# Optimization experiments

Hardware: AMD Instinct MI355X
Metric: run time of the kernel (lower is better)

Reference implementation:

```python
import jax, jax.numpy as jnp
import numpy as np

B, V, P, D = 32, 6, 197, 512
L = 77          # CLIP token length
C = 5           # num quality perspectives (conditions)

def _normalize(x, axis=-1, eps=1e-12):
    n = jnp.linalg.norm(x, axis=axis, keepdims=True)
    return x / jnp.maximum(n, eps)

def _conv3x3(x, w, b):
    # x: [C,112,7,7], w: [O,112,3,3] -> [C,O,7,7]
    y = jax.lax.conv_general_dilated(x, w, (1, 1), 'SAME',
                                     dimension_numbers=('NCHW', 'OIHW', 'NCHW'))
    return y + b[None, :, None, None]

def setup_inputs() -> dict:
    key = jax.random.key(0)
    ks = jax.random.split(key, 20)
    s = 0.02  # weight init scale keeps sigmoids in linear-ish range
    return {
        'feature_texture': jax.random.normal(ks[0], (B, V * P, D), jnp.float32),
        'feature_prompt': jax.random.normal(ks[1], (B, L, D), jnp.float32),
        'feature_prompt_eot': jax.random.normal(ks[2], (B, D), jnp.float32),
        'feature_condition': jax.random.normal(ks[3], (C, D), jnp.float32),
        'fc_quality_w': jax.random.normal(ks[4], (224, D), jnp.float32) * s,
        'fc_quality_b': jnp.zeros((224,), jnp.float32),
        'fc_condition_w': jax.random.normal(ks[5], (5488, D), jnp.float32) * s,
        'fc_condition_b': jnp.zeros((5488,), jnp.float32),
        'fc1w_conv_w': jax.random.normal(ks[6], (512, 112, 3, 3), jnp.float32) * s,
        'fc1w_conv_b': jnp.zeros((512,), jnp.float32),
        'fc2w_conv_w': jax.random.normal(ks[7], (128, 112, 3, 3), jnp.float32) * s,
        'fc2w_conv_b': jnp.zeros((128,), jnp.float32),
        'fc3w_conv_w': jax.random.normal(ks[8], (32, 112, 3, 3), jnp.float32) * s,
        'fc3w_conv_b': jnp.zeros((32,), jnp.float32),
        'fc4w_conv_w': jax.random.normal(ks[9], (8, 112, 3, 3), jnp.float32) * s,
        'fc4w_conv_b': jnp.zeros((8,), jnp.float32),
        'fc1b_w': jax.random.normal(ks[10], (112, 112), jnp.float32) * s,
        'fc1b_b': jnp.zeros((112,), jnp.float32),
        'fc2b_w': jax.random.normal(ks[11], (56, 112), jnp.float32) * s,
        'fc2b_b': jnp.zeros((56,), jnp.float32),
        'fc3b_w': jax.random.normal(ks[12], (28, 112), jnp.float32) * s,
        'fc3b_b': jnp.zeros((28,), jnp.float32),
        'fc4b_w': jax.random.normal(ks[13], (14, 112), jnp.float32) * s,
        'fc4b_b': jnp.zeros((14,), jnp.float32),
        'fc5w_w': jax.random.normal(ks[14], (14, 112), jnp.float32) * s,
        'fc5w_b': jnp.zeros((14,), jnp.float32),
        'fc5b_w': jax.random.normal(ks[15], (1, 112), jnp.float32) * s,
        'fc5b_b': jnp.zeros((1,), jnp.float32),
    }

def reference(feature_texture, feature_prompt, feature_prompt_eot, feature_condition,
              fc_quality_w, fc_quality_b, fc_condition_w, fc_condition_b,
              fc1w_conv_w, fc1w_conv_b, fc2w_conv_w, fc2w_conv_b,
              fc3w_conv_w, fc3w_conv_b, fc4w_conv_w, fc4w_conv_b,
              fc1b_w, fc1b_b, fc2b_w, fc2b_b, fc3b_w, fc3b_b, fc4b_w, fc4b_b,
              fc5w_w, fc5w_b, fc5b_w, fc5b_b):
    nC = feature_condition.shape[0]

    # --- calculate_cos: mean of relu(pairwise cosine sim), upper triangle i<j ---
    fn = _normalize(feature_condition)                      # [C,512]
    gram = fn @ fn.T                                        # [C,C]
    iu, ju = jnp.triu_indices(nC, k=1)
    loss_dis = jnp.mean(jnp.maximum(gram[iu, ju], 0.0))

    # --- cross-attention-style patch weighting ---
    np_prompt = _normalize(feature_prompt, axis=2)          # [B,L,D]
    np_tex = _normalize(feature_texture, axis=2)            # [B,J,D]
    sim_texture = jnp.einsum('bid,bjd->bji', np_prompt, np_tex)   # [B,J,L]
    sim_cond = jnp.einsum('bid,cd->bci', np_prompt, fn)           # [B,C,L]
    patch_weight = jnp.einsum('bcl,bjl->bjc', sim_cond, sim_texture)  # [B,J,C]
    patch_weight = jax.nn.softmax(patch_weight, axis=1)

    # --- condition feature maps for hypernet: [C,112,7,7] ---
    cond_maps = (feature_condition @ fc_condition_w.T + fc_condition_b)
    cond_maps = cond_maps.reshape(nC, 112, 7, 7)

    # --- hypernet: generate TargetNet params for all conditions at once ---
    pooled = cond_maps.mean(axis=(2, 3))                              # [C,112]
    fc1w = _conv3x3(cond_maps, fc1w_conv_w, fc1w_conv_b).reshape(nC, 112, 224)
    fc2w = _conv3x3(cond_maps, fc2w_conv_w, fc2w_conv_b).reshape(nC, 56, 112)
    fc3w = _conv3x3(cond_maps, fc3w_conv_w, fc3w_conv_b).reshape(nC, 28, 56)
    fc4w = _conv3x3(cond_maps, fc4w_conv_w, fc4w_conv_b).reshape(nC, 14, 28)
    fc1b = pooled @ fc1b_w.T + fc1b_b                                 # [C,112]
    fc2b = pooled @ fc2b_w.T + fc2b_b                                 # [C,56]
    fc3b = pooled @ fc3b_w.T + fc3b_b                                 # [C,28]
    fc4b = pooled @ fc4b_w.T + fc4b_b                                 # [C,14]
    fc5w = pooled @ fc5w_w.T + fc5w_b                                 # [C,14]
    fc5b = pooled @ fc5b_w.T + fc5b_b                                 # [C,1]

    # --- fused quality feature per (batch, condition) ---
    ftf = jnp.einsum('bjd,bjc->bcd', feature_texture, patch_weight)   # [B,C,D]
    fused = ftf * feature_prompt_eot[:, None, :]                      # [B,C,D]
    fq = jnp.einsum('bcd,kd->bck', fused, fc_quality_w) + fc_quality_b  # [B,C,224]

    # --- TargetNet (per-condition generated weights), vectorized over loop ---
    h = jax.nn.sigmoid(jnp.einsum('bck,cjk->bcj', fq, fc1w) + fc1b[None])
    h = jax.nn.sigmoid(jnp.einsum('bcj,cij->bci', h, fc2w) + fc2b[None])
    h = jax.nn.sigmoid(jnp.einsum('bci,coi->bco', h, fc3w) + fc3b[None])
    h = jax.nn.sigmoid(jnp.einsum('bco,cpo->bcp', h, fc4w) + fc4b[None])
    score_list = jnp.einsum('bcp,cp->bc', h, fc5w) + fc5b[:, 0][None]  # [B,C]

    return score_list, loss_dis
```

## Files before the change

### kernel.cpp

```cpp
#include <hip/hip_runtime.h>
#include <hip/hip_bf16.h>
#include <math.h>

#define B_   32
#define J_   1182
#define D_   512
#define L_   77
#define C_   5
#define JC_  64
#define NCH_ 19
#define NPW_ 74
#define JPW_ 16

__device__ __forceinline__ float dot4(float4 a, float4 b) {
    return a.x*b.x + a.y*b.y + a.z*b.z + a.w*b.w;
}

__device__ __forceinline__ float wave_sum(float v) {
#pragma unroll
    for (int off = 32; off > 0; off >>= 1) v += __shfl_xor(v, off, 64);
    return v;
}

__device__ __forceinline__ float wave_max(float v) {
#pragma unroll
    for (int off = 32; off > 0; off >>= 1) v = fmaxf(v, __shfl_xor(v, off, 64));
    return v;
}

__global__ void k_front(const float* __restrict__ fc, const float* __restrict__ cw,
                        const float* __restrict__ cb, float* __restrict__ cm,
                        float* __restrict__ loss_out,
                        const float* __restrict__ fp, float* __restrict__ swl) {
    __shared__ float4 smem4[640];
    float* sfc = (float*)smem4;
    int bid = blockIdx.x, t = threadIdx.x;
    int wave = t >> 6, lane = t & 63;

    if (bid < 1373) {
        for (int i = t; i < C_*D_; i += 256) sfc[i] = fc[i];
        __syncthreads();

        if (bid == 1372) {
            for (int c = wave; c < C_; c += 4) {
                float ss = 0.f;
                for (int d = lane; d < D_; d += 64) { float v = sfc[c*D_+d]; ss += v*v; }
                ss = wave_sum(ss);
                float inv = 1.f / fmaxf(sqrtf(ss), 1e-12f);
                for (int d = lane; d < D_; d += 64) sfc[c*D_+d] *= inv;
            }
            __syncthreads();
            if (wave == 0) {
                float acc = 0.f;
                for (int i = 0; i < C_; ++i)
                    for (int j = i+1; j < C_; ++j) {
                        float p = 0.f;
                        for (int d = lane; d < D_; d += 64) p += sfc[i*D_+d]*sfc[j*D_+d];
                        p = wave_sum(p);
                        acc += fmaxf(p, 0.f);
                    }
                if (lane == 0) *loss_out = acc * (1.f/10.f);
            }
            return;
        }

        int o = bid*4 + wave;
        const float4* w4 = (const float4*)(cw + (size_t)o*D_);
        float4 wa = w4[lane], wb = w4[lane+64];
        float bias = cb[o];
        float keep = 0.f;
#pragma unroll
        for (int c = 0; c < C_; ++c) {
            const float4* f4 = (const float4*)(sfc + c*D_);
            float s = dot4(wa, f4[lane]) + dot4(wb, f4[lane+64]);
            s = wave_sum(s);
            if (lane == c) keep = s;
        }
        if (lane < C_) cm[lane*5488 + o] = keep + bias;
        return;
    }

    for (int c = wave; c < C_; c += 4) {
        const float4* f8 = (const float4*)(fc + c*D_);
        float4 v0 = f8[lane*2], v1 = f8[lane*2+1];
        float ss = dot4(v0,v0) + dot4(v1,v1);
        ss = wave_sum(ss);
        float inv = 1.f / fmaxf(sqrtf(ss), 1e-12f);
        v0.x*=inv; v0.y*=inv; v0.z*=inv; v0.w*=inv;
        v1.x*=inv; v1.y*=inv; v1.z*=inv; v1.w*=inv;
        int f0 = lane*2, f1 = lane*2+1;
        smem4[(c*16 + (f0 & 15))*8 + (f0 >> 4)] = v0;
        smem4[(c*16 + (f1 & 15))*8 + (f1 >> 4)] = v1;
    }
    __syncthreads();

    int row = t >> 3, seg = t & 7;
    int bl = (bid - 1373)*32 + row;
    int b = bl / L_, l = bl - b*L_;
    const float4* p4 = ((const float4*)(fp + (size_t)bl*D_)) + seg*16;
    float ss=0.f, s0=0.f, s1=0.f, s2=0.f, s3=0.f, s4=0.f;
#pragma unroll 4
    for (int k = 0; k < 16; ++k) {
        float4 v = p4[k];
        int base = k*8 + seg;
        ss += dot4(v, v);
        s0 += dot4(v, smem4[base]);
        s1 += dot4(v, smem4[128 + base]);
        s2 += dot4(v, smem4[256 + base]);
        s3 += dot4(v, smem4[384 + base]);
        s4 += dot4(v, smem4[512 + base]);
    }
#pragma unroll
    for (int off = 1; off < 8; off <<= 1) {
        ss += __shfl_xor(ss,off,64);
        s0 += __shfl_xor(s0,off,64); s1 += __shfl_xor(s1,off,64);
        s2 += __shfl_xor(s2,off,64); s3 += __shfl_xor(s3,off,64);
        s4 += __shfl_xor(s4,off,64);
    }
    if (seg == 0) {
        float inv = 1.f / fmaxf(sqrtf(ss), 1e-12f);
        float inv2 = inv*inv;
        swl[((size_t)(b*C_+0))*L_ + l] = s0*inv2;
        swl[((size_t)(b*C_+1))*L_ + l] = s1*inv2;
        swl[((size_t)(b*C_+2))*L_ + l] = s2*inv2;
        swl[((size_t)(b*C_+3))*L_ + l] = s3*inv2;
        swl[((size_t)(b*C_+4))*L_ + l] = s4*inv2;
    }
}

__global__ void k_Q(const float* __restrict__ fp, const float* __restrict__ swl,
                    float* __restrict__ Q) {
    __shared__ float sw[C_][80];
    int b = blockIdx.y;
    int t = threadIdx.x;
    for (int i = t; i < C_*L_; i += 256) { int c = i/L_, l = i - c*L_; sw[c][l] = swl[((size_t)(b*C_+c))*L_ + l]; }
    __syncthreads();
    int d = blockIdx.x*256 + t;
    float a0=0.f, a1=0.f, a2=0.f, a3=0.f, a4=0.f;
    const float* f = fp + (size_t)b*L_*D_ + d;
    for (int l = 0; l < L_; ++l) {
        float v = f[(size_t)l*D_];
        a0 += sw[0][l]*v; a1 += sw[1][l]*v; a2 += sw[2][l]*v;
        a3 += sw[3][l]*v; a4 += sw[4][l]*v;
    }
    Q[(size_t)(b*C_+0)*D_ + d] = a0;
    Q[(size_t)(b*C_+1)*D_ + d] = a1;
    Q[(size_t)(b*C_+2)*D_ + d] = a2;
    Q[(size_t)(b*C_+3)*D_ + d] = a3;
    Q[(size_t)(b*C_+4)*D_ + d] = a4;
}

__global__ void k_conv_pw(const float* __restrict__ cm,
                          const float* __restrict__ w1, const float* __restrict__ bb1,
                          const float* __restrict__ w2, const float* __restrict__ bb2,
                          const float* __restrict__ w3, const float* __restrict__ bb3,
                          const float* __restrict__ w4, const float* __restrict__ bb4,
                          float* __restrict__ o1, float* __restrict__ o2,
                          float* __restrict__ o3, float* __restrict__ o4,
                          const float* __restrict__ w1b, const float* __restrict__ b1b,
                          const float* __restrict__ w2b, const float* __restrict__ b2b,
                          const float* __restrict__ w3b, const float* __restrict__ b3b,
                          const float* __restrict__ w4b, const float* __restrict__ b4b,
                          const float* __restrict__ w5w, const float* __restrict__ b5w,
                          const float* __restrict__ w5b, const float* __restrict__ b5b,
                          float* __restrict__ fcb,
                          const float* __restrict__ tex, const float* __restrict__ Q,
                          float* __restrict__ pw, float2* __restrict__ pstat) {
    __shared__ float smem[12352];
    int bid = blockIdx.x;
    int t = threadIdx.x;

    if (bid >= 375) {
        float* stex = smem;
        float* sq   = smem + 9216;
        float* srawT = smem + 12096;
        int p = bid - 375;
        int bx = p % NPW_, b = p / NPW_;
        int j0 = bx*JPW_;
        int jn = min(JPW_, J_ - j0);

        {
            const float4* q4 = (const float4*)(Q + (size_t)b*C_*D_);
            for (int i = t; i < C_*128; i += 256) {
                int c = i >> 7, col4 = i & 127;
                *(float4*)(sq + c*576 + col4*4 + ((col4>>3)<<2)) = q4[i];
            }
            const float4* t4 = (const float4*)(tex + ((size_t)(b*J_ + j0))*D_);
#pragma unroll
            for (int n = 0; n < 8; ++n) {
                int i = n*256 + t;
                int row = i >> 7, col4 = i & 127;
                if (row < jn)
                    *(float4*)(stex + row*576 + col4*4 + ((col4>>3)<<2)) = t4[i];
            }
        }
        __syncthreads();

        {
            int row = t >> 4, seg = t & 15;
            const float* sr = stex + row*576;
            float ss=0.f, s0=0.f, s1=0.f, s2=0.f, s3=0.f, s4=0.f;
#pragma unroll
            for (int k = 0; k < 8; ++k) {
                int col4 = seg*8 + k;
                int wa = col4*4 + ((col4>>3)<<2);
                float4 v = *(const float4*)(sr + wa);
                ss += dot4(v, v);
                s0 += dot4(v, *(const float4*)(sq +          wa));
                s1 += dot4(v, *(const float4*)(sq +   576 + wa));
                s2 += dot4(v, *(const float4*)(sq + 2*576 + wa));
                s3 += dot4(v, *(const float4*)(sq + 3*576 + wa));
                s4 += dot4(v, *(const float4*)(sq + 4*576 + wa));
            }
#pragma unroll
            for (int off = 1; off < 16; off <<= 1) {
                ss += __shfl_xor(ss,off,64);
                s0 += __shfl_xor(s0,off,64); s1 += __shfl_xor(s1,off,64);
                s2 += __shfl_xor(s2,off,64); s3 += __shfl_xor(s3,off,64);
                s4 += __shfl_xor(s4,off,64);
            }
            if (seg == 0) {
                if (row < jn) {
                    float inv = 1.f / fmaxf(sqrtf(ss), 1e-12f);
                    float r0=s0*inv, r1=s1*inv, r2=s2*inv, r3=s3*inv, r4=s4*inv;
                    int j = j0 + row;
                    pw[((size_t)(b*C_+0))*J_ + j] = r0;
                    pw[((size_t)(b*C_+1))*J_ + j] = r1;
                    pw[((size_t)(b*C_+2))*J_ + j] = r2;
                    pw[((size_t)(b*C_+3))*J_ + j] = r3;
                    pw[((size_t)(b*C_+4))*J_ + j] = r4;
                    srawT[row*8+0]=r0; srawT[row*8+1]=r1; srawT[row*8+2]=r2;
                    srawT[row*8+3]=r3; srawT[row*8+4]=r4;
                } else {
                    srawT[row*8+0]=-1e30f; srawT[row*8+1]=-1e30f; srawT[row*8+2]=-1e30f;
                    srawT[row*8+3]=-1e30f; srawT[row*8+4]=-1e30f;
                }
            }
        }
        __syncthreads();

        {
            int wave = t >> 6, lane = t & 63;
            bool act = (wave == 0) || (wave == 1 && lane < 16);
            if (act) {
                int c = (wave == 0) ? (lane >> 4) : 4;
                int row = lane & 15;
                float v = srawT[row*8+c];
                float m = v;
#pragma unroll
                for (int off = 1; off < 16; off <<= 1) m = fmaxf(m, __shfl_xor(m,off,64));
                float e = (row < jn) ? expf(v - m) : 0.f;
                float s = e;
#pragma unroll
                for (int off = 1; off < 16; off <<= 1) s += __shfl_xor(s,off,64);
                if (row == 0) pstat[(size_t)(bx*B_+b)*C_ + c] = make_float2(m, s);
            }
        }
        return;
    }

    float* im = smem;
    float* sp = smem + 12096;
    int c  = bid / 75;
    int bx = bid - c*75;
    for (int i = t; i < 112*108; i += 256) im[i] = 0.f;
    __syncthreads();
    const float* cmc = cm + c*5488;
    for (int i = t; i < 112*49; i += 256) {
        int ch = i / 49, yx = i - ch*49;
        int y = yx / 7, x = yx - y*7;
        im[ch*108 + (y+1)*12 + (x+1)] = cmc[i];
    }
    __syncthreads();

    if (bx == 0) {
        if (t < 112) {
            const float* p = im + t*108;
            float s = 0.f;
            for (int k = 0; k < 108; ++k) s += p[k];
            sp[t] = s * (1.f/49.f);
        }
        __syncthreads();
        if (t < 225) {
            int rel = t;
            const float* w; const float* bb; int nout; int base;
            if      (rel < 112) {            w=w1b; bb=b1b; nout=112; base=0; }
            else if (rel < 168) { rel-=112;  w=w2b; bb=b2b; nout=56;  base=560; }
            else if (rel < 196) { rel-=168;  w=w3b; bb=b3b; nout=28;  base=840; }
            else if (rel < 210) { rel-=196;  w=w4b; bb=b4b; nout=14;  base=980; }
            else if (rel < 224) { rel-=210;  w=w5w; bb=b5w; nout=14;  base=1050; }
            else                { rel-=224;  w=w5b; bb=b5b; nout=1;   base=1120; }
            float s = bb[rel];
            const float* wr = w + rel*112;
            for (int i = 0; i < 112; ++i) s += sp[i]*wr[i];
            fcb[base + c*nout + rel] = s;
        }
    }

    int oyl = t & 63;
    int chq = t >> 6;
    int oy  = bx*64 + oyl;
    int oyc = (oy < 4760) ? oy : 0;
    int o_comb = oyc / 7, y = oyc - o_comb*7;
    const float* w; int o;
    if      (o_comb < 512) { w=w1; o=o_comb; }
    else if (o_comb < 640) { w=w2; o=o_comb-512; }
    else if (o_comb < 672) { w=w3; o=o_comb-640; }
    else                   { w=w4; o=o_comb-672; }

    float ac0=0,ac1=0,ac2=0,ac3=0,ac4=0,ac5=0,ac6=0;
    const float* wbase = w + ((size_t)o*112 + chq*28)*9;
    const float* imc   = im + (chq*28)*108 + y*12;
#pragma unroll 2
    for (int ch = 0; ch < 28; ++ch) {
        const float* wk = wbase + ch*9;
        const float* ii = imc + ch*108;
        float w0=wk[0],w1_=wk[1],w2_=wk[2],w3_=wk[3],w4_=wk[4],w5_=wk[5],w6_=wk[6],w7_=wk[7],w8_=wk[8];
#pragma unroll
        for (int ky = 0; ky < 3; ++ky) {
            const float* row = ii + ky*12;
            float4 ra = *(const float4*)(row);
            float4 rb = *(const float4*)(row + 4);
            float  rc = row[8];
            float r0=ra.x,r1=ra.y,r2=ra.z,r3=ra.w,r4=rb.x,r5=rb.y,r6=rb.z,r7=rb.w,r8=rc;
            float wk0 = (ky==0)?w0:((ky==1)?w3_:w6_);
            float wk1 = (ky==0)?w1_:((ky==1)?w4_:w7_);
            float wk2 = (ky==0)?w2_:((ky==1)?w5_:w8_);
            ac0 += r0*wk0 + r1*wk1 + r2*wk2;
            ac1 += r1*wk0 + r2*wk1 + r3*wk2;
            ac2 += r2*wk0 + r3*wk1 + r4*wk2;
            ac3 += r3*wk0 + r4*wk1 + r5*wk2;
            ac4 += r4*wk0 + r5*wk1 + r6*wk2;
            ac5 += r5*wk0 + r6*wk1 + r7*wk2;
            ac6 += r6*wk0 + r7*wk1 + r8*wk2;
        }
    }
    __syncthreads();
    float* partb = im;
    {
        int pb = (chq*64 + oyl)*9;
        partb[pb+0]=ac0; partb[pb+1]=ac1; partb[pb+2]=ac2; partb[pb+3]=ac3;
        partb[pb+4]=ac4; partb[pb+5]=ac5; partb[pb+6]=ac6;
    }
    __syncthreads();
    for (int i = t; i < 448; i += 256) {
        int oyl2 = i / 7, x = i - oyl2*7;
        int oy2 = bx*64 + oyl2;
        if (oy2 < 4760) {
            float s = partb[(0*64+oyl2)*9+x] + partb[(1*64+oyl2)*9+x]
                    + partb[(2*64+oyl2)*9+x] + partb[(3*64+oyl2)*9+x];
            int oc = oy2/7, yy = oy2 - oc*7;
            const float* bias; float* outp; int oo;
            if      (oc < 512) { bias=bb1; outp=o1 + (size_t)c*512*49; oo=oc; }
            else if (oc < 640) { bias=bb2; outp=o2 + (size_t)c*128*49; oo=oc-512; }
            else if (oc < 672) { bias=bb3; outp=o3 + (size_t)c*32*49;  oo=oc-640; }
            else               { bias=bb4; outp=o4 + (size_t)c*8*49;   oo=oc-672; }
            outp[oo*49 + yy*7 + x] = s + bias[oo];
        }
    }
}

__global__ void k_ftf(const float* __restrict__ tex, const float* __restrict__ pwraw,
                      const float2* __restrict__ pstat, float* __restrict__ part) {
    __shared__ float sw[C_][JC_];
    __shared__ float2 sL[C_];
    int chunk = blockIdx.x, b = blockIdx.y;
    int t = threadIdx.x;
    int wave = t >> 6, lane = t & 63;
    if (wave < C_) {
        float2 pa = (lane < NPW_) ? pstat[(size_t)(lane*B_ + b)*C_ + wave]
                                  : make_float2(-1e30f, 0.f);
        float2 pb = (lane+64 < NPW_) ? pstat[(size_t)((lane+64)*B_ + b)*C_ + wave]
                                     : make_float2(-1e30f, 0.f);
        float m = wave_max(fmaxf(pa.x, pb.x));
        float contrib = pa.y * expf(pa.x - m) + pb.y * expf(pb.x - m);
        float denom = wave_sum(contrib);
        if (lane == 0) sL[wave] = make_float2(m, 1.f/denom);
    }
    __syncthreads();
    int j0 = chunk*JC_;
    int jn = min(JC_, J_ - j0);
    if (t < C_*JC_) {
        int c = t >> 6, jj = t & 63;
        float2 ms = sL[c];
        sw[c][jj] = (jj < jn)
            ? expf(pwraw[((size_t)(b*C_+c))*J_ + j0 + jj] - ms.x) * ms.y
            : 0.f;
    }
    __syncthreads();
    float acc0=0.f, acc1=0.f, acc2=0.f, acc3=0.f, acc4=0.f;
    const float* tp = tex + ((size_t)b*J_ + j0)*D_ + t;
    for (int jj = 0; jj < jn; ++jj) {
        float v = tp[(size_t)jj*D_];
        acc0 += v*sw[0][jj]; acc1 += v*sw[1][jj]; acc2 += v*sw[2][jj];
        acc3 += v*sw[3][jj]; acc4 += v*sw[4][jj];
    }
    size_t base = (((size_t)chunk*B_ + b)*C_)*D_ + t;
    part[base               ] = acc0;
    part[base +   (size_t)D_] = acc1;
    part[base + 2*(size_t)D_] = acc2;
    part[base + 3*(size_t)D_] = acc3;
    part[base + 4*(size_t)D_] = acc4;
}

__global__ void k_fq_target(const float* __restrict__ part, const float* __restrict__ eot,
                            const float* __restrict__ qw, const float* __restrict__ qb,
                            const float* __restrict__ g1w, const float* __restrict__ g2w,
                            const float* __restrict__ g3w, const float* __restrict__ g4w,
                            const float* __restrict__ fcb, float* __restrict__ out) {
    int bc = blockIdx.x; int b = bc / C_; int c = bc - b*C_;
    __shared__ float sf[D_];
    __shared__ float sa[224], sb[112];
    int t = threadIdx.x;

    float s0 = 0.f, s1 = 0.f;
    for (int ch = 0; ch < NCH_; ++ch) {
        const float* p = part + ((size_t)ch*(B_*C_) + bc)*D_;
        s0 += p[t]; s1 += p[t+256];
    }
    sf[t]     = s0 * eot[b*D_ + t];
    sf[t+256] = s1 * eot[b*D_ + t + 256];
    __syncthreads();

    if (t < 224) {
        const float4* w4 = (const float4*)(qw + (size_t)t*D_);
        const float4* s4 = (const float4*)sf;
        float acc = 0.f;
#pragma unroll 4
        for (int i = 0; i < 128; ++i) acc += dot4(s4[i], w4[i]);
        sa[t] = acc + qb[t];
    }
    __syncthreads();

    if (t < 112) {
        const float* w = g1w + (size_t)c*25088 + t*224;
        float s = fcb[c*112 + t];
        for (int k = 0; k < 224; ++k) s += w[k]*sa[k];
        sb[t] = 1.f/(1.f+expf(-s));
    }
    __syncthreads();
    if (t < 56) {
        const float* w = g2w + (size_t)c*6272 + t*112;
        float s = fcb[560 + c*56 + t];
        for (int k = 0; k < 112; ++k) s += w[k]*sb[k];
        sa[t] = 1.f/(1.f+expf(-s));
    }
    __syncthreads();
    if (t < 28) {
        const float* w = g3w + (size_t)c*1568 + t*56;
        float s = fcb[840 + c*28 + t];
        for (int k = 0; k < 56; ++k) s += w[k]*sa[k];
        sb[t] = 1.f/(1.f+expf(-s));
    }
    __syncthreads();
    if (t < 14) {
        const float* w = g4w + (size_t)c*392 + t*28;
        float s = fcb[980 + c*14 + t];
        for (int k = 0; k < 28; ++k) s += w[k]*sb[k];
        sa[t] = 1.f/(1.f+expf(-s));
    }
    __syncthreads();
    if (t == 0) {
        float s = fcb[1120 + c];
        for (int p = 0; p < 14; ++p) s += sa[p]*fcb[1050 + c*14 + p];
        out[b*C_ + c] = s;
    }
}

extern "C" void kernel_launch(void* const* d_in, const int* in_sizes, int n_in,
                              void* d_out, int out_size, void* d_ws, size_t ws_size,
                              hipStream_t stream) {
    (void)in_sizes; (void)n_in; (void)out_size; (void)ws_size;
    const float* tex   = (const float*)d_in[0];
    const float* fp    = (const float*)d_in[1];
    const float* eot   = (const float*)d_in[2];
    const float* fcond = (const float*)d_in[3];
    const float* qw    = (const float*)d_in[4];
    const float* qb    = (const float*)d_in[5];
    const float* cw    = (const float*)d_in[6];
    const float* cb    = (const float*)d_in[7];
    const float* w1c   = (const float*)d_in[8];  const float* b1c = (const float*)d_in[9];
    const float* w2c   = (const float*)d_in[10]; const float* b2c = (const float*)d_in[11];
    const float* w3c   = (const float*)d_in[12]; const float* b3c = (const float*)d_in[13];
    const float* w4c   = (const float*)d_in[14]; const float* b4c = (const float*)d_in[15];
    const float* f1bw  = (const float*)d_in[16]; const float* f1bb = (const float*)d_in[17];
    const float* f2bw  = (const float*)d_in[18]; const float* f2bb = (const float*)d_in[19];
    const float* f3bw  = (const float*)d_in[20]; const float* f3bb = (const float*)d_in[21];
    const float* f4bw  = (const float*)d_in[22]; const float* f4bb = (const float*)d_in[23];
    const float* f5ww  = (const float*)d_in[24]; const float* f5wb = (const float*)d_in[25];
    const float* f5bw  = (const float*)d_in[26]; const float* f5bb = (const float*)d_in[27];
    float* out = (float*)d_out;

    float* ws     = (float*)d_ws;
    float* Qb     = ws;
    float* pw     = Qb + 81920;
    float* part   = pw + 189120;
    float* pstat  = part + 1556480;
    float* cm     = pstat + 23680;
    float* g1w    = cm + 27440;
    float* g2w    = g1w + 125440;
    float* g3w    = g2w + 31360;
    float* g4w    = g3w + 7840;
    float* fcb    = g4w + 1960;
    float* swl    = fcb + 1125;

    k_front<<<1450, 256, 0, stream>>>(fcond, cw, cb, cm, out + B_*C_, fp, swl);
    k_Q<<<dim3(2, B_), 256, 0, stream>>>(fp, swl, Qb);
    k_conv_pw<<<375 + NPW_*B_, 256, 0, stream>>>(cm, w1c, b1c, w2c, b2c, w3c, b3c, w4c, b4c,
                                        g1w, g2w, g3w, g4w,
                                        f1bw, f1bb, f2bw, f2bb, f3bw, f3bb,
                                        f4bw, f4bb, f5ww, f5wb, f5bw, f5bb, fcb,
                                        tex, Qb, pw, (float2*)pstat);
    k_ftf<<<dim3(NCH_, B_), 512, 0, stream>>>(tex, pw, (const float2*)pstat, part);
    k_fq_target<<<B_*C_, 256, 0, stream>>>(part, eot, qw, qb,
                                           g1w, g2w, g3w, g4w, fcb, out);
}
```

Measured before the change: 90.54 us.

## Move conv weight generation into ftf kernel and split patch-weight pass

The conv weight-generation blocks used to share a launch with the patch-weight cosine pass. They now share a launch with the softmax-weighted texture reduction (ftf), and the patch-weight pass becomes its own kernel. The shared block size goes to 512 threads, so the conv path splits channels into 8 groups of 14 instead of 4 of 28 and sums 8 partials. The aim is to overlap the conv work with the longer ftf reduction rather than with the shorter pw pass, and to give the conv blocks more parallelism. The cost is a different shared-memory footprint and occupancy for the merged kernel.

```diff
diff --git a/kernel.cpp b/kernel.cpp
--- a/kernel.cpp
+++ b/kernel.cpp
@@ -150,112 +150,157 @@
     Q[(size_t)(b*C_+4)*D_ + d] = a4;
 }
 
-__global__ void k_conv_pw(const float* __restrict__ cm,
-                          const float* __restrict__ w1, const float* __restrict__ bb1,
-                          const float* __restrict__ w2, const float* __restrict__ bb2,
-                          const float* __restrict__ w3, const float* __restrict__ bb3,
-                          const float* __restrict__ w4, const float* __restrict__ bb4,
-                          float* __restrict__ o1, float* __restrict__ o2,
-                          float* __restrict__ o3, float* __restrict__ o4,
-                          const float* __restrict__ w1b, const float* __restrict__ b1b,
-                          const float* __restrict__ w2b, const float* __restrict__ b2b,
-                          const float* __restrict__ w3b, const float* __restrict__ b3b,
-                          const float* __restrict__ w4b, const float* __restrict__ b4b,
-                          const float* __restrict__ w5w, const float* __restrict__ b5w,
-                          const float* __restrict__ w5b, const float* __restrict__ b5b,
-                          float* __restrict__ fcb,
-                          const float* __restrict__ tex, const float* __restrict__ Q,
-                          float* __restrict__ pw, float2* __restrict__ pstat) {
-    __shared__ float smem[12352];
+__global__ void k_pw(const float* __restrict__ tex, const float* __restrict__ Q,
+                     float* __restrict__ pw, float2* __restrict__ pstat) {
+    __shared__ float smem[12224];
+    float* stex = smem;
+    float* sq   = smem + 9216;
+    float* srawT = smem + 12096;
+    int p = blockIdx.x;
+    int bx = p % NPW_, b = p / NPW_;
+    int t = threadIdx.x;
+    int j0 = bx*JPW_;
+    int jn = min(JPW_, J_ - j0);
+
+    {
+        const float4* q4 = (const float4*)(Q + (size_t)b*C_*D_);
+        for (int i = t; i < C_*128; i += 256) {
+            int c = i >> 7, col4 = i & 127;
+            *(float4*)(sq + c*576 + col4*4 + ((col4>>3)<<2)) = q4[i];
+        }
+        const float4* t4 = (const float4*)(tex + ((size_t)(b*J_ + j0))*D_);
+#pragma unroll
+        for (int n = 0; n < 8; ++n) {
+            int i = n*256 + t;
+            int row = i >> 7, col4 = i & 127;
+            if (row < jn)
+                *(float4*)(stex + row*576 + col4*4 + ((col4>>3)<<2)) = t4[i];
+        }
+    }
+    __syncthreads();
+
+    {
+        int row = t >> 4, seg = t & 15;
+        const float* sr = stex + row*576;
+        float ss=0.f, s0=0.f, s1=0.f, s2=0.f, s3=0.f, s4=0.f;
+#pragma unroll
+        for (int k = 0; k < 8; ++k) {
+            int col4 = seg*8 + k;
+            int wa = col4*4 + ((col4>>3)<<2);
+            float4 v = *(const float4*)(sr + wa);
+            ss += dot4(v, v);
+            s0 += dot4(v, *(const float4*)(sq +          wa));
+            s1 += dot4(v, *(const float4*)(sq +   576 + wa));
+            s2 += dot4(v, *(const float4*)(sq + 2*576 + wa));
+            s3 += dot4(v, *(const float4*)(sq + 3*576 + wa));
+            s4 += dot4(v, *(const float4*)(sq + 4*576 + wa));
+        }
+#pragma unroll
+        for (int off = 1; off < 16; off <<= 1) {
+            ss += __shfl_xor(ss,off,64);
+            s0 += __shfl_xor(s0,off,64); s1 += __shfl_xor(s1,off,64);
+            s2 += __shfl_xor(s2,off,64); s3 += __shfl_xor(s3,off,64);
+            s4 += __shfl_xor(s4,off,64);
+        }
+        if (seg == 0) {
+            if (row < jn) {
+                float inv = 1.f / fmaxf(sqrtf(ss), 1e-12f);
+                float r0=s0*inv, r1=s1*inv, r2=s2*inv, r3=s3*inv, r4=s4*inv;
+                int j = j0 + row;
+                pw[((size_t)(b*C_+0))*J_ + j] = r0;
+                pw[((size_t)(b*C_+1))*J_ + j] = r1;
+                pw[((size_t)(b*C_+2))*J_ + j] = r2;
+                pw[((size_t)(b*C_+3))*J_ + j] = r3;
+                pw[((size_t)(b*C_+4))*J_ + j] = r4;
+                srawT[row*8+0]=r0; srawT[row*8+1]=r1; srawT[row*8+2]=r2;
+                srawT[row*8+3]=r3; srawT[row*8+4]=r4;
+            } else {
+                srawT[row*8+0]=-1e30f; srawT[row*8+1]=-1e30f; srawT[row*8+2]=-1e30f;
+                srawT[row*8+3]=-1e30f; srawT[row*8+4]=-1e30f;
+            }
+        }
+    }
+    __syncthreads();
+
+    {
+        int wave = t >> 6, lane = t & 63;
+        bool act = (wave == 0) || (wave == 1 && lane < 16);
+        if (act) {
+            int c = (wave == 0) ? (lane >> 4) : 4;
+            int row = lane & 15;
+            float v = srawT[row*8+c];
+            float m = v;
+#pragma unroll
+            for (int off = 1; off < 16; off <<= 1) m = fmaxf(m, __shfl_xor(m,off,64));
+            float e = (row < jn) ? expf(v - m) : 0.f;
+            float s = e;
+#pragma unroll
+            for (int off = 1; off < 16; off <<= 1) s += __shfl_xor(s,off,64);
+            if (row == 0) pstat[(size_t)(bx*B_+b)*C_ + c] = make_float2(m, s);
+        }
+    }
+}
+
+__global__ void k_ftf_conv(const float* __restrict__ tex, const float* __restrict__ pwraw,
+                           const float2* __restrict__ pstat, float* __restrict__ part,
+                           const float* __restrict__ cm,
+                           const float* __restrict__ w1, const float* __restrict__ bb1,
+                           const float* __restrict__ w2, const float* __restrict__ bb2,
+                           const float* __restrict__ w3, const float* __restrict__ bb3,
+                           const float* __restrict__ w4, const float* __restrict__ bb4,
+                           float* __restrict__ o1, float* __restrict__ o2,
+                           float* __restrict__ o3, float* __restrict__ o4,
+                           const float* __restrict__ w1b, const float* __restrict__ b1b,
+                           const float* __restrict__ w2b, const float* __restrict__ b2b,
+                           const float* __restrict__ w3b, const float* __restrict__ b3b,
+                           const float* __restrict__ w4b, const float* __restrict__ b4b,
+                           const float* __restrict__ w5w, const float* __restrict__ b5w,
+                           const float* __restrict__ w5b, const float* __restrict__ b5b,
+                           float* __restrict__ fcb) {
+    __shared__ float smem[12208];
     int bid = blockIdx.x;
     int t = threadIdx.x;
 
     if (bid >= 375) {
-        float* stex = smem;
-        float* sq   = smem + 9216;
-        float* srawT = smem + 12096;
+        float* swv = smem;
+        float2* sL = (float2*)(smem + 320);
         int p = bid - 375;
-        int bx = p % NPW_, b = p / NPW_;
-        int j0 = bx*JPW_;
-        int jn = min(JPW_, J_ - j0);
-
-        {
-            const float4* q4 = (const float4*)(Q + (size_t)b*C_*D_);
-            for (int i = t; i < C_*128; i += 256) {
-                int c = i >> 7, col4 = i & 127;
-                *(float4*)(sq + c*576 + col4*4 + ((col4>>3)<<2)) = q4[i];
-            }
-            const float4* t4 = (const float4*)(tex + ((size_t)(b*J_ + j0))*D_);
-#pragma unroll
-            for (int n = 0; n < 8; ++n) {
-                int i = n*256 + t;
-                int row = i >> 7, col4 = i & 127;
-                if (row < jn)
-                    *(float4*)(stex + row*576 + col4*4 + ((col4>>3)<<2)) = t4[i];
-            }
+        int chunk = p % NCH_, b = p / NCH_;
+        int wave = t >> 6, lane = t & 63;
+        if (wave < C_) {
+            float2 pa = (lane < NPW_) ? pstat[(size_t)(lane*B_ + b)*C_ + wave]
+                                      : make_float2(-1e30f, 0.f);
+            float2 pb = (lane+64 < NPW_) ? pstat[(size_t)((lane+64)*B_ + b)*C_ + wave]
+                                         : make_float2(-1e30f, 0.f);
+            float m = wave_max(fmaxf(pa.x, pb.x));
+            float contrib = pa.y * expf(pa.x - m) + pb.y * expf(pb.x - m);
+            float denom = wave_sum(contrib);
+            if (lane == 0) sL[wave] = make_float2(m, 1.f/denom);
         }
         __syncthreads();
-
-        {
-            int row = t >> 4, seg = t & 15;
-            const float* sr = stex + row*576;
-            float ss=0.f, s0=0.f, s1=0.f, s2=0.f, s3=0.f, s4=0.f;
-#pragma unroll
-            for (int k = 0; k < 8; ++k) {
-                int col4 = seg*8 + k;
-                int wa = col4*4 + ((col4>>3)<<2);
-                float4 v = *(const float4*)(sr + wa);
-                ss += dot4(v, v);
-                s0 += dot4(v, *(const float4*)(sq +          wa));
-                s1 += dot4(v, *(const float4*)(sq +   576 + wa));
-                s2 += dot4(v, *(const float4*)(sq + 2*576 + wa));
-                s3 += dot4(v, *(const float4*)(sq + 3*576 + wa));
-                s4 += dot4(v, *(const float4*)(sq + 4*576 + wa));
-            }
-#pragma unroll
-            for (int off = 1; off < 16; off <<= 1) {
-                ss += __shfl_xor(ss,off,64);
-                s0 += __shfl_xor(s0,off,64); s1 += __shfl_xor(s1,off,64);
-                s2 += __shfl_xor(s2,off,64); s3 += __shfl_xor(s3,off,64);
-                s4 += __shfl_xor(s4,off,64);
-            }
-            if (seg == 0) {
-                if (row < jn) {
-                    float inv = 1.f / fmaxf(sqrtf(ss), 1e-12f);
-                    float r0=s0*inv, r1=s1*inv, r2=s2*inv, r3=s3*inv, r4=s4*inv;
-                    int j = j0 + row;
-                    pw[((size_t)(b*C_+0))*J_ + j] = r0;
-                    pw[((size_t)(b*C_+1))*J_ + j] = r1;
-                    pw[((size_t)(b*C_+2))*J_ + j] = r2;
-                    pw[((size_t)(b*C_+3))*J_ + j] = r3;
-                    pw[((size_t)(b*C_+4))*J_ + j] = r4;
-                    srawT[row*8+0]=r0; srawT[row*8+1]=r1; srawT[row*8+2]=r2;
-                    srawT[row*8+3]=r3; srawT[row*8+4]=r4;
-                } else {
-                    srawT[row*8+0]=-1e30f; srawT[row*8+1]=-1e30f; srawT[row*8+2]=-1e30f;
-                    srawT[row*8+3]=-1e30f; srawT[row*8+4]=-1e30f;
-                }
-            }
+        int j0 = chunk*JC_;
+        int jn = min(JC_, J_ - j0);
+        if (t < C_*JC_) {
+            int c = t >> 6, jj = t & 63;
+            float2 ms = sL[c];
+            swv[c*JC_+jj] = (jj < jn)
+                ? expf(pwraw[((size_t)(b*C_+c))*J_ + j0 + jj] - ms.x) * ms.y
+                : 0.f;
         }
         __syncthreads();
-
-        {
-            int wave = t >> 6, lane = t & 63;
-            bool act = (wave == 0) || (wave == 1 && lane < 16);
-            if (act) {
-                int c = (wave == 0) ? (lane >> 4) : 4;
-                int row = lane & 15;
-                float v = srawT[row*8+c];
-                float m = v;
-#pragma unroll
-                for (int off = 1; off < 16; off <<= 1) m = fmaxf(m, __shfl_xor(m,off,64));
-                float e = (row < jn) ? expf(v - m) : 0.f;
-                float s = e;
-#pragma unroll
-                for (int off = 1; off < 16; off <<= 1) s += __shfl_xor(s,off,64);
-                if (row == 0) pstat[(size_t)(bx*B_+b)*C_ + c] = make_float2(m, s);
-            }
-        }
+        float acc0=0.f, acc1=0.f, acc2=0.f, acc3=0.f, acc4=0.f;
+        const float* tp = tex + ((size_t)b*J_ + j0)*D_ + t;
+        for (int jj = 0; jj < jn; ++jj) {
+            float v = tp[(size_t)jj*D_];
+            acc0 += v*swv[0*JC_+jj]; acc1 += v*swv[1*JC_+jj]; acc2 += v*swv[2*JC_+jj];
+            acc3 += v*swv[3*JC_+jj]; acc4 += v*swv[4*JC_+jj];
+        }
+        size_t base = (((size_t)chunk*B_ + b)*C_)*D_ + t;
+        part[base               ] = acc0;
+        part[base +   (size_t)D_] = acc1;
+        part[base + 2*(size_t)D_] = acc2;
+        part[base + 3*(size_t)D_] = acc3;
+        part[base + 4*(size_t)D_] = acc4;
         return;
     }
 
@@ -263,10 +308,10 @@
     float* sp = smem + 12096;
     int c  = bid / 75;
     int bx = bid - c*75;
-    for (int i = t; i < 112*108; i += 256) im[i] = 0.f;
+    for (int i = t; i < 112*108; i += 512) im[i] = 0.f;
     __syncthreads();
     const float* cmc = cm + c*5488;
-    for (int i = t; i < 112*49; i += 256) {
+    for (int i = t; i < 112*49; i += 512) {
         int ch = i / 49, yx = i - ch*49;
         int y = yx / 7, x = yx - y*7;
         im[ch*108 + (y+1)*12 + (x+1)] = cmc[i];
@@ -309,10 +354,10 @@
     else                   { w=w4; o=o_comb-672; }
 
     float ac0=0,ac1=0,ac2=0,ac3=0,ac4=0,ac5=0,ac6=0;
-    const float* wbase = w + ((size_t)o*112 + chq*28)*9;
-    const float* imc   = im + (chq*28)*108 + y*12;
+    const float* wbase = w + ((size_t)o*112 + chq*14)*9;
+    const float* imc   = im + (chq*14)*108 + y*12;
 #pragma unroll 2
-    for (int ch = 0; ch < 28; ++ch) {
+    for (int ch = 0; ch < 14; ++ch) {
         const float* wk = wbase + ch*9;
         const float* ii = imc + ch*108;
         float w0=wk[0],w1_=wk[1],w2_=wk[2],w3_=wk[3],w4_=wk[4],w5_=wk[5],w6_=wk[6],w7_=wk[7],w8_=wk[8];
@@ -343,12 +388,13 @@
         partb[pb+4]=ac4; partb[pb+5]=ac5; partb[pb+6]=ac6;
     }
     __syncthreads();
-    for (int i = t; i < 448; i += 256) {
-        int oyl2 = i / 7, x = i - oyl2*7;
+    if (t < 448) {
+        int oyl2 = t / 7, x = t - oyl2*7;
         int oy2 = bx*64 + oyl2;
         if (oy2 < 4760) {
-            float s = partb[(0*64+oyl2)*9+x] + partb[(1*64+oyl2)*9+x]
-                    + partb[(2*64+oyl2)*9+x] + partb[(3*64+oyl2)*9+x];
+            float s = 0.f;
+#pragma unroll
+            for (int q = 0; q < 8; ++q) s += partb[(q*64+oyl2)*9+x];
             int oc = oy2/7, yy = oy2 - oc*7;
             const float* bias; float* outp; int oo;
             if      (oc < 512) { bias=bb1; outp=o1 + (size_t)c*512*49; oo=oc; }
@@ -358,49 +404,6 @@
             outp[oo*49 + yy*7 + x] = s + bias[oo];
         }
     }
-}
-
-__global__ void k_ftf(const float* __restrict__ tex, const float* __restrict__ pwraw,
-                      const float2* __restrict__ pstat, float* __restrict__ part) {
-    __shared__ float sw[C_][JC_];
-    __shared__ float2 sL[C_];
-    int chunk = blockIdx.x, b = blockIdx.y;
-    int t = threadIdx.x;
-    int wave = t >> 6, lane = t & 63;
-    if (wave < C_) {
-        float2 pa = (lane < NPW_) ? pstat[(size_t)(lane*B_ + b)*C_ + wave]
-                                  : make_float2(-1e30f, 0.f);
-        float2 pb = (lane+64 < NPW_) ? pstat[(size_t)((lane+64)*B_ + b)*C_ + wave]
-                                     : make_float2(-1e30f, 0.f);
-        float m = wave_max(fmaxf(pa.x, pb.x));
-        float contrib = pa.y * expf(pa.x - m) + pb.y * expf(pb.x - m);
-        float denom = wave_sum(contrib);
-        if (lane == 0) sL[wave] = make_float2(m, 1.f/denom);
-    }
-    __syncthreads();
-    int j0 = chunk*JC_;
-    int jn = min(JC_, J_ - j0);
-    if (t < C_*JC_) {
-        int c = t >> 6, jj = t & 63;
-        float2 ms = sL[c];
-        sw[c][jj] = (jj < jn)
-            ? expf(pwraw[((size_t)(b*C_+c))*J_ + j0 + jj] - ms.x) * ms.y
-            : 0.f;
-    }
-    __syncthreads();
-    float acc0=0.f, acc1=0.f, acc2=0.f, acc3=0.f, acc4=0.f;
-    const float* tp = tex + ((size_t)b*J_ + j0)*D_ + t;
-    for (int jj = 0; jj < jn; ++jj) {
-        float v = tp[(size_t)jj*D_];
-        acc0 += v*sw[0][jj]; acc1 += v*sw[1][jj]; acc2 += v*sw[2][jj];
-        acc3 += v*sw[3][jj]; acc4 += v*sw[4][jj];
-    }
-    size_t base = (((size_t)chunk*B_ + b)*C_)*D_ + t;
-    part[base               ] = acc0;
-    part[base +   (size_t)D_] = acc1;
-    part[base + 2*(size_t)D_] = acc2;
-    part[base + 3*(size_t)D_] = acc3;
-    part[base + 4*(size_t)D_] = acc4;
 }
 
 __global__ void k_fq_target(const float* __restrict__ part, const float* __restrict__ eot,
@@ -506,12 +509,12 @@
 
     k_front<<<1450, 256, 0, stream>>>(fcond, cw, cb, cm, out + B_*C_, fp, swl);
     k_Q<<<dim3(2, B_), 256, 0, stream>>>(fp, swl, Qb);
-    k_conv_pw<<<375 + NPW_*B_, 256, 0, stream>>>(cm, w1c, b1c, w2c, b2c, w3c, b3c, w4c, b4c,
+    k_pw<<<NPW_*B_, 256, 0, stream>>>(tex, Qb, pw, (float2*)pstat);
+    k_ftf_conv<<<375 + NCH_*B_, 512, 0, stream>>>(tex, pw, (const float2*)pstat, part,
+                                        cm, w1c, b1c, w2c, b2c, w3c, b3c, w4c, b4c,
                                         g1w, g2w, g3w, g4w,
                                         f1bw, f1bb, f2bw, f2bb, f3bw, f3bb,
-                                        f4bw, f4bb, f5ww, f5wb, f5bw, f5bb, fcb,
-                                        tex, Qb, pw, (float2*)pstat);
-    k_ftf<<<dim3(NCH_, B_), 512, 0, stream>>>(tex, pw, (const float2*)pstat, part);
+                                        f4bw, f4bb, f5ww, f5wb, f5bw, f5bb, fcb);
     k_fq_target<<<B_*C_, 256, 0, stream>>>(part, eot, qw, qb,
                                            g1w, g2w, g3w, g4w, fcb, out);
 }
```

Measured after the change: 92.02 us. About the same (+1.6%).
